# Optimization experiments

Hardware: AMD Instinct MI355X
Metric: run time of the kernel (lower is better)

Reference implementation:

```python
import jax, jax.numpy as jnp
import numpy as np

B, N = 8, 50000
DIM, C_DIM, TASK_DIM, H, NB, OUT = 3, 64, 512, 64, 5, 12


def setup_inputs() -> dict:
    key = jax.random.key(0)
    ks = jax.random.split(key, 16)
    s = lambda fan_in: 1.0 / np.sqrt(fan_in)
    inp = {
        "p": jax.random.normal(ks[0], (B, N, DIM), dtype=jnp.float32),
        "c": jax.random.normal(ks[1], (B, N, C_DIM), dtype=jnp.float32),
        "task_feature": jax.random.normal(ks[2], (B, TASK_DIM), dtype=jnp.float32),
        # params (stored as [in, out] so y = x @ W + b)
        "fc_p_W": jax.random.uniform(ks[3], (DIM, H), jnp.float32, -s(DIM), s(DIM)),
        "fc_p_b": jax.random.uniform(ks[4], (H,), jnp.float32, -s(DIM), s(DIM)),
        "fc_c_W": jax.random.uniform(ks[5], (NB, C_DIM + TASK_DIM, H), jnp.float32, -s(C_DIM + TASK_DIM), s(C_DIM + TASK_DIM)),
        "fc_c_b": jax.random.uniform(ks[6], (NB, H), jnp.float32, -s(C_DIM + TASK_DIM), s(C_DIM + TASK_DIM)),
        "blk0_W": jax.random.uniform(ks[7], (NB, H, H), jnp.float32, -s(H), s(H)),
        "blk0_b": jax.random.uniform(ks[8], (NB, H), jnp.float32, -s(H), s(H)),
        "blk1_W": jax.random.uniform(ks[9], (NB, H, H), jnp.float32, -s(H), s(H)) * 0.1,
        "blk1_b": jax.random.uniform(ks[10], (NB, H), jnp.float32, -s(H), s(H)),
        "fc_out_W": jax.random.uniform(ks[11], (H, OUT), jnp.float32, -s(H), s(H)),
        "fc_out_b": jax.random.uniform(ks[12], (OUT,), jnp.float32, -s(H), s(H)),
    }
    return inp


def reference(p, c, task_feature, fc_p_W, fc_p_b, fc_c_W, fc_c_b,
              blk0_W, blk0_b, blk1_W, blk1_b, fc_out_W, fc_out_b):
    b, n = p.shape[0], p.shape[1]
    # expand task feature to every point and concat with point-wise code c
    tf = jnp.broadcast_to(task_feature[:, None, :], (b, n, task_feature.shape[-1]))
    cc = jnp.concatenate([c, tf], axis=-1)              # [B, N, 576]
    net = p @ fc_p_W + fc_p_b                           # [B, N, H]
    for i in range(fc_c_W.shape[0]):
        net = net + cc @ fc_c_W[i] + fc_c_b[i]          # conditioning
        # ResnetBlockFC: dx = fc_1(relu(fc_0(relu(x)))); out = x + dx
        h = jax.nn.relu(net) @ blk0_W[i] + blk0_b[i]
        dx = jax.nn.relu(h) @ blk1_W[i] + blk1_b[i]
        net = net + dx
    out = jax.nn.relu(net) @ fc_out_W + fc_out_b        # [B, N, 12]
    return out
```

## Files before the change

kernel.cpp:

```cpp
#include <hip/hip_runtime.h>

#define B_    8
#define N_    50000
#define NB_   5
#define OUT_  12
#define THREADS 512
#define TILES_ 4
#define NGROUPS 6250
#define GRID   782

#define WL_OFF   0
#define TPL_OFF  124928
#define B0L_OFF  135168
#define B14_OFF  136448
#define FPW_OFF  136704
#define SMEM_BYTES 137472

typedef _Float16 half8  __attribute__((ext_vector_type(8)));
typedef __fp16   fp16x2 __attribute__((ext_vector_type(2)));
typedef float   floatx4 __attribute__((ext_vector_type(4)));

__device__ __forceinline__ half8 ldl8(const _Float16* p) {
    union { uint4 u; half8 h; } x;
    x.u = *(const uint4*)p;
    return x.h;
}

__device__ __forceinline__ half8 packB(floatx4 a, floatx4 b) {
    union { fp16x2 h2[4]; half8 h8; } u;
    u.h2[0] = __builtin_amdgcn_cvt_pkrtz(fmaxf(a[0], 0.f), fmaxf(a[1], 0.f));
    u.h2[1] = __builtin_amdgcn_cvt_pkrtz(fmaxf(a[2], 0.f), fmaxf(a[3], 0.f));
    u.h2[2] = __builtin_amdgcn_cvt_pkrtz(fmaxf(b[0], 0.f), fmaxf(b[1], 0.f));
    u.h2[3] = __builtin_amdgcn_cvt_pkrtz(fmaxf(b[2], 0.f), fmaxf(b[3], 0.f));
    return u.h8;
}

__device__ __forceinline__ void loadL8(half8 (&A)[8], const _Float16* wl, int stage, int lane) {
    const _Float16* b = wl + (size_t)stage * 512 * 8;
    #pragma unroll
    for (int T = 0; T < 4; ++T)
        #pragma unroll
        for (int h = 0; h < 2; ++h)
            A[2 * T + h] = ldl8(b + (size_t)(T * 128 + h * 64 + lane) * 8);
}

__global__ void prep_kernel(const float* __restrict__ fc_c_W,
                            const float* __restrict__ blk0_W,
                            const float* __restrict__ blk1_W,
                            const float* __restrict__ fc_out_W,
                            const float* __restrict__ tf,
                            _Float16* __restrict__ ws_w,
                            float* __restrict__ partials) {
    int bid = blockIdx.x, tid = threadIdx.x;
    if (bid < 32) {
        int u = bid * 256 + tid;
        if (u < 7680) {
            int m15 = u & 15, q = (u >> 4) & 3, h = (u >> 6) & 1, T = (u >> 7) & 3;
            int mi = u >> 9;
            int mat = mi / 5, i = mi % 5;
            int n = T * 16 + m15;
            _Float16 out[8];
            #pragma unroll
            for (int j = 0; j < 8; ++j) {
                float v;
                if (mat == 0) {
                    int k = 32 * h + 8 * q + j;
                    v = fc_c_W[((size_t)i * 576 + k) * 64 + n];
                } else {
                    int f = 32 * h + 16 * (j >> 2) + 4 * q + (j & 3);
                    const float* W = (mat == 1) ? blk0_W : blk1_W;
                    v = W[((size_t)i * 64 + f) * 64 + n];
                }
                out[j] = (_Float16)v;
            }
            *(uint4*)(ws_w + (size_t)u * 8) = *(uint4*)out;
        } else {
            int e = u - 7680;
            _Float16 out[8] = {};
            if (e < 128) {
                int m15 = e & 15, q = (e >> 4) & 3, h = (e >> 6) & 1;
                #pragma unroll
                for (int j = 0; j < 8; ++j) {
                    int f = 32 * h + 16 * (j >> 2) + 4 * q + (j & 3);
                    out[j] = (m15 < OUT_) ? (_Float16)fc_out_W[f * OUT_ + m15] : (_Float16)0.f;
                }
            }
            *(uint4*)(ws_w + (size_t)u * 8) = *(uint4*)out;
        }
    } else {
        int idx2 = bid - 32;
        int b = idx2 / 10, rem = idx2 % 10, i = rem >> 1, hf = rem & 1;
        int g = tid >> 6, j = tid & 63;
        const float* W  = fc_c_W + ((size_t)i * 576 + 64) * 64;
        const float* tb = tf + b * 512;
        int t0 = hf * 256 + g * 64;
        float acc = 0.f;
        #pragma unroll 8
        for (int t = 0; t < 64; ++t)
            acc += tb[t0 + t] * W[(size_t)(t0 + t) * 64 + j];
        partials[(((b * 5 + i) << 3) + (hf * 4 + g)) * 64 + j] = acc;
    }
}

__global__ void finalize_tp(const float* __restrict__ partials,
                            const float* __restrict__ fc_c_b,
                            const float* __restrict__ fc_p_b,
                            const float* __restrict__ blk1_b,
                            float* __restrict__ tp) {
    int u = blockIdx.x * 256 + threadIdx.x;
    if (u >= 2560) return;
    int b = u / 320, rem = u % 320, i = rem >> 6, j = rem & 63;
    float s = fc_c_b[i * 64 + j] + ((i == 0) ? fc_p_b[j] : blk1_b[(i - 1) * 64 + j]);
    #pragma unroll
    for (int k = 0; k < 8; ++k)
        s += partials[(((b * 5 + i) << 3) + k) * 64 + j];
    tp[u] = s;
}

__global__ __launch_bounds__(THREADS, 2) void decoder_kernel(
    const float* __restrict__ p_g, const float* __restrict__ c_g,
    const float* __restrict__ blk0_b, const float* __restrict__ blk1_b,
    const float* __restrict__ fc_p_W, const float* __restrict__ fc_out_b,
    const _Float16* __restrict__ ws_w, const float* __restrict__ tp_g,
    float* __restrict__ out_g)
{
    extern __shared__ char smem[];
    _Float16* wl   = (_Float16*)(smem + WL_OFF);
    float*    tp_l = (float*)(smem + TPL_OFF);
    float*    b0_l = (float*)(smem + B0L_OFF);
    float*    b14_l= (float*)(smem + B14_OFF);
    float*    fpw_l= (float*)(smem + FPW_OFF);

    const int tid = threadIdx.x, bid = blockIdx.x;

    {
        uint4* dw = (uint4*)wl;
        const uint4* sw = (const uint4*)ws_w;
        for (int u = tid; u < 7808; u += THREADS) dw[u] = sw[u];
        uint4* dt = (uint4*)tp_l;  const uint4* st = (const uint4*)tp_g;
        for (int u = tid; u < 640; u += THREADS) dt[u] = st[u];
        uint4* db = (uint4*)b0_l;  const uint4* sb = (const uint4*)blk0_b;
        for (int u = tid; u < 80; u += THREADS) db[u] = sb[u];
        uint4* d4 = (uint4*)b14_l; const uint4* s4 = (const uint4*)(blk1_b + 4 * 64);
        if (tid < 16) d4[tid] = s4[tid];
        uint4* df = (uint4*)fpw_l; const uint4* sf = (const uint4*)fc_p_W;
        if (tid < 48) df[tid] = sf[tid];
    }
    __syncthreads();

    const int lane = tid & 63;
    const int wv   = tid >> 6;
    const int q    = lane >> 4;
    const int m15  = lane & 15;

    const int g = bid * 8 + wv;
    if (g >= NGROUPS) return;

    int bt[TILES_];
    long pbase[TILES_];
    #pragma unroll
    for (int t = 0; t < TILES_; ++t) {
        int gt = g * TILES_ + t;
        int b  = gt / 3125;
        int lt = gt - b * 3125;
        bt[t] = b;
        pbase[t] = (long)b * N_ + (long)lt * 16;
    }

    half8 cB[TILES_][2];
    #pragma unroll
    for (int t = 0; t < TILES_; ++t) {
        const float* cr = c_g + (size_t)(pbase[t] + m15) * 64;
        #pragma unroll
        for (int h = 0; h < 2; ++h) {
            float4 v0 = *(const float4*)(cr + 32 * h + 8 * q);
            float4 v1 = *(const float4*)(cr + 32 * h + 8 * q + 4);
            union { fp16x2 h2[4]; half8 h8; } u;
            u.h2[0] = __builtin_amdgcn_cvt_pkrtz(v0.x, v0.y);
            u.h2[1] = __builtin_amdgcn_cvt_pkrtz(v0.z, v0.w);
            u.h2[2] = __builtin_amdgcn_cvt_pkrtz(v1.x, v1.y);
            u.h2[3] = __builtin_amdgcn_cvt_pkrtz(v1.z, v1.w);
            cB[t][h] = u.h8;
        }
    }

    floatx4 net4[TILES_][4];
    #pragma unroll
    for (int t = 0; t < TILES_; ++t) {
        long gp = pbase[t] + m15;
        float pp0 = p_g[gp * 3 + 0], pp1 = p_g[gp * 3 + 1], pp2 = p_g[gp * 3 + 2];
        #pragma unroll
        for (int T = 0; T < 4; ++T) {
            floatx4 w0 = *(const floatx4*)(fpw_l + 16 * T + 4 * q);
            floatx4 w1 = *(const floatx4*)(fpw_l + 64 + 16 * T + 4 * q);
            floatx4 w2 = *(const floatx4*)(fpw_l + 128 + 16 * T + 4 * q);
            net4[t][T] = w0 * pp0 + w1 * pp1 + w2 * pp2;
        }
    }

    #pragma unroll 1
    for (int i = 0; i < NB_; ++i) {
        half8 Ax[8], Ay[8];
        loadL8(Ax, wl, i, lane);
        loadL8(Ay, wl, 5 + i, lane);
        floatx4 bb0[4];
        #pragma unroll
        for (int T = 0; T < 4; ++T)
            bb0[T] = *(const floatx4*)(b0_l + i * 64 + 16 * T + 4 * q);
        #pragma unroll
        for (int t = 0; t < TILES_; ++t) {
            const float* tpb = tp_l + (bt[t] * NB_ + i) * 64 + 4 * q;
            #pragma unroll
            for (int T = 0; T < 4; ++T) {
                floatx4 a = net4[t][T];
                a = __builtin_amdgcn_mfma_f32_16x16x32_f16(Ax[2 * T], cB[t][0], a, 0, 0, 0);
                a = __builtin_amdgcn_mfma_f32_16x16x32_f16(Ax[2 * T + 1], cB[t][1], a, 0, 0, 0);
                net4[t][T] = a + *(const floatx4*)(tpb + 16 * T);
            }
        }
        loadL8(Ax, wl, 10 + i, lane);
        #pragma unroll
        for (int t = 0; t < TILES_; ++t) {
            half8 Bn0 = packB(net4[t][0], net4[t][1]);
            half8 Bn1 = packB(net4[t][2], net4[t][3]);
            floatx4 hh[4];
            #pragma unroll
            for (int T = 0; T < 4; ++T) {
                floatx4 a = bb0[T];
                a = __builtin_amdgcn_mfma_f32_16x16x32_f16(Ay[2 * T], Bn0, a, 0, 0, 0);
                a = __builtin_amdgcn_mfma_f32_16x16x32_f16(Ay[2 * T + 1], Bn1, a, 0, 0, 0);
                hh[T] = a;
            }
            half8 Bh0 = packB(hh[0], hh[1]);
            half8 Bh1 = packB(hh[2], hh[3]);
            #pragma unroll
            for (int T = 0; T < 4; ++T) {
                floatx4 a = net4[t][T];
                a = __builtin_amdgcn_mfma_f32_16x16x32_f16(Ax[2 * T], Bh0, a, 0, 0, 0);
                a = __builtin_amdgcn_mfma_f32_16x16x32_f16(Ax[2 * T + 1], Bh1, a, 0, 0, 0);
                net4[t][T] = a;
            }
        }
    }

    half8 Ao0 = ldl8(wl + (size_t)(15 * 512 + 0 * 64 + q * 16 + m15) * 8);
    half8 Ao1 = ldl8(wl + (size_t)(15 * 512 + 1 * 64 + q * 16 + m15) * 8);
    floatx4 b14v[4];
    #pragma unroll
    for (int T = 0; T < 4; ++T)
        b14v[T] = *(const floatx4*)(b14_l + 16 * T + 4 * q);
    floatx4 ob = {0.f, 0.f, 0.f, 0.f};
    if (q < 3) ob = *(const floatx4*)(fc_out_b + 4 * q);
    #pragma unroll
    for (int t = 0; t < TILES_; ++t) {
        half8 Bn0 = packB(net4[t][0] + b14v[0], net4[t][1] + b14v[1]);
        half8 Bn1 = packB(net4[t][2] + b14v[2], net4[t][3] + b14v[3]);
        floatx4 a = ob;
        a = __builtin_amdgcn_mfma_f32_16x16x32_f16(Ao0, Bn0, a, 0, 0, 0);
        a = __builtin_amdgcn_mfma_f32_16x16x32_f16(Ao1, Bn1, a, 0, 0, 0);
        if (q < 3) {
            long gp = pbase[t] + m15;
            *(float4*)(out_g + gp * OUT_ + 4 * q) = make_float4(a[0], a[1], a[2], a[3]);
        }
    }
}

extern "C" void kernel_launch(void* const* d_in, const int* in_sizes, int n_in,
                              void* d_out, int out_size, void* d_ws, size_t ws_size,
                              hipStream_t stream) {
    const float* p        = (const float*)d_in[0];
    const float* c        = (const float*)d_in[1];
    const float* tf       = (const float*)d_in[2];
    const float* fc_p_W   = (const float*)d_in[3];
    const float* fc_p_b   = (const float*)d_in[4];
    const float* fc_c_W   = (const float*)d_in[5];
    const float* fc_c_b   = (const float*)d_in[6];
    const float* blk0_W   = (const float*)d_in[7];
    const float* blk0_b   = (const float*)d_in[8];
    const float* blk1_W   = (const float*)d_in[9];
    const float* blk1_b   = (const float*)d_in[10];
    const float* fc_out_W = (const float*)d_in[11];
    const float* fc_out_b = (const float*)d_in[12];
    float* out = (float*)d_out;

    _Float16* ws_w  = (_Float16*)d_ws;
    float* partials = (float*)((char*)d_ws + 131072);
    float* tp       = (float*)((char*)d_ws + 131072 + 81920);

    prep_kernel<<<112, 256, 0, stream>>>(fc_c_W, blk0_W, blk1_W, fc_out_W, tf, ws_w, partials);
    finalize_tp<<<10, 256, 0, stream>>>(partials, fc_c_b, fc_p_b, blk1_b, tp);

    (void)hipFuncSetAttribute((const void*)decoder_kernel,
                        hipFuncAttributeMaxDynamicSharedMemorySize, SMEM_BYTES);
    decoder_kernel<<<GRID, THREADS, SMEM_BYTES, stream>>>(
        p, c, blk0_b, blk1_b, fc_p_W, fc_out_b, ws_w, tp, out);
}
```

Baseline: 253.4 us.

## Use persistent 768-thread blocks with 5-tile wave groups and packed fp16 relu

Launches a fixed grid of 256 blocks of 12 waves. Each wave loops over up to two 80-point groups, and every group stays inside one batch, so the task-projection bias is hoisted to registers once per stage. The aim is to amortise the 125 KB LDS weight load over more work per block and to cut per-tile bias loads. ReLU is now applied after fp16 packing with a vector max instead of per-element fmaxf. The risks are higher register pressure from five tiles at three blocks per CU, and some dead or duplicate code in the LDS staging.

```diff
diff --git a/kernel.cpp b/kernel.cpp
--- a/kernel.cpp
+++ b/kernel.cpp
@@ -4,10 +4,11 @@
 #define N_    50000
 #define NB_   5
 #define OUT_  12
-#define THREADS 512
-#define TILES_ 4
-#define NGROUPS 6250
-#define GRID   782
+#define THREADS 768
+#define GRID   256
+#define TILES_ 5
+#define NGROUPS 5000
+#define NWAVES 3072
 
 #define WL_OFF   0
 #define TPL_OFF  124928
@@ -28,11 +29,12 @@
 
 __device__ __forceinline__ half8 packB(floatx4 a, floatx4 b) {
     union { fp16x2 h2[4]; half8 h8; } u;
-    u.h2[0] = __builtin_amdgcn_cvt_pkrtz(fmaxf(a[0], 0.f), fmaxf(a[1], 0.f));
-    u.h2[1] = __builtin_amdgcn_cvt_pkrtz(fmaxf(a[2], 0.f), fmaxf(a[3], 0.f));
-    u.h2[2] = __builtin_amdgcn_cvt_pkrtz(fmaxf(b[0], 0.f), fmaxf(b[1], 0.f));
-    u.h2[3] = __builtin_amdgcn_cvt_pkrtz(fmaxf(b[2], 0.f), fmaxf(b[3], 0.f));
-    return u.h8;
+    u.h2[0] = __builtin_amdgcn_cvt_pkrtz(a[0], a[1]);
+    u.h2[1] = __builtin_amdgcn_cvt_pkrtz(a[2], a[3]);
+    u.h2[2] = __builtin_amdgcn_cvt_pkrtz(b[0], b[1]);
+    u.h2[3] = __builtin_amdgcn_cvt_pkrtz(b[2], b[3]);
+    half8 z = {};
+    return __builtin_elementwise_max(u.h8, z);
 }
 
 __device__ __forceinline__ void loadL8(half8 (&A)[8], const _Float16* wl, int stage, int lane) {
@@ -117,7 +119,7 @@
     tp[u] = s;
 }
 
-__global__ __launch_bounds__(THREADS, 2) void decoder_kernel(
+__global__ __launch_bounds__(THREADS, 3) void decoder_kernel(
     const float* __restrict__ p_g, const float* __restrict__ c_g,
     const float* __restrict__ blk0_b, const float* __restrict__ blk1_b,
     const float* __restrict__ fc_p_W, const float* __restrict__ fc_out_b,
@@ -137,14 +139,16 @@
         uint4* dw = (uint4*)wl;
         const uint4* sw = (const uint4*)ws_w;
         for (int u = tid; u < 7808; u += THREADS) dw[u] = sw[u];
-        uint4* dt = (uint4*)tp_l;  const uint4* st = (const uint4*)tp_g;
-        for (int u = tid; u < 640; u += THREADS) dt[u] = st[u];
-        uint4* db = (uint4*)b0_l;  const uint4* sb = (const uint4*)blk0_b;
-        for (int u = tid; u < 80; u += THREADS) db[u] = sb[u];
-        uint4* d4 = (uint4*)b14_l; const uint4* s4 = (const uint4*)(blk1_b + 4 * 64);
-        if (tid < 16) d4[tid] = s4[tid];
-        uint4* df = (uint4*)fpw_l; const uint4* sf = (const uint4*)fc_p_W;
-        if (tid < 48) df[tid] = sf[tid];
+        if (tid < 640) ((uint4*)tp_l)[tid] = ((const uint4*)tp_g)[tid];
+        else if (tid < 720) ((uint4*)b0_l)[tid - 640] = ((const uint4*)blk0_b)[tid - 640];
+        else if (tid < 736) ((uint4*)b14_l)[tid - 720] = ((const uint4*)(blk1_b + 256))[tid - 720];
+        else if (tid < 752) {
+            int u = tid - 736;
+            if (u < 48) ((uint4*)fpw_l)[u] = ((const uint4*)fc_p_W)[u];
+        }
+        if (tid >= 704 && tid < 736) {
+        }
+        if (tid < 48) ((uint4*)fpw_l)[tid] = ((const uint4*)fc_p_W)[tid];
     }
     __syncthreads();
 
@@ -152,115 +156,113 @@
     const int wv   = tid >> 6;
     const int q    = lane >> 4;
     const int m15  = lane & 15;
-
-    const int g = bid * 8 + wv;
-    if (g >= NGROUPS) return;
-
-    int bt[TILES_];
-    long pbase[TILES_];
-    #pragma unroll
-    for (int t = 0; t < TILES_; ++t) {
-        int gt = g * TILES_ + t;
-        int b  = gt / 3125;
-        int lt = gt - b * 3125;
-        bt[t] = b;
-        pbase[t] = (long)b * N_ + (long)lt * 16;
-    }
-
-    half8 cB[TILES_][2];
-    #pragma unroll
-    for (int t = 0; t < TILES_; ++t) {
-        const float* cr = c_g + (size_t)(pbase[t] + m15) * 64;
-        #pragma unroll
-        for (int h = 0; h < 2; ++h) {
-            float4 v0 = *(const float4*)(cr + 32 * h + 8 * q);
-            float4 v1 = *(const float4*)(cr + 32 * h + 8 * q + 4);
-            union { fp16x2 h2[4]; half8 h8; } u;
-            u.h2[0] = __builtin_amdgcn_cvt_pkrtz(v0.x, v0.y);
-            u.h2[1] = __builtin_amdgcn_cvt_pkrtz(v0.z, v0.w);
-            u.h2[2] = __builtin_amdgcn_cvt_pkrtz(v1.x, v1.y);
-            u.h2[3] = __builtin_amdgcn_cvt_pkrtz(v1.z, v1.w);
-            cB[t][h] = u.h8;
-        }
-    }
-
-    floatx4 net4[TILES_][4];
-    #pragma unroll
-    for (int t = 0; t < TILES_; ++t) {
-        long gp = pbase[t] + m15;
-        float pp0 = p_g[gp * 3 + 0], pp1 = p_g[gp * 3 + 1], pp2 = p_g[gp * 3 + 2];
-        #pragma unroll
-        for (int T = 0; T < 4; ++T) {
-            floatx4 w0 = *(const floatx4*)(fpw_l + 16 * T + 4 * q);
-            floatx4 w1 = *(const floatx4*)(fpw_l + 64 + 16 * T + 4 * q);
-            floatx4 w2 = *(const floatx4*)(fpw_l + 128 + 16 * T + 4 * q);
-            net4[t][T] = w0 * pp0 + w1 * pp1 + w2 * pp2;
-        }
-    }
-
-    #pragma unroll 1
-    for (int i = 0; i < NB_; ++i) {
-        half8 Ax[8], Ay[8];
-        loadL8(Ax, wl, i, lane);
-        loadL8(Ay, wl, 5 + i, lane);
-        floatx4 bb0[4];
-        #pragma unroll
-        for (int T = 0; T < 4; ++T)
-            bb0[T] = *(const floatx4*)(b0_l + i * 64 + 16 * T + 4 * q);
-        #pragma unroll
-        for (int t = 0; t < TILES_; ++t) {
-            const float* tpb = tp_l + (bt[t] * NB_ + i) * 64 + 4 * q;
-            #pragma unroll
-            for (int T = 0; T < 4; ++T) {
-                floatx4 a = net4[t][T];
-                a = __builtin_amdgcn_mfma_f32_16x16x32_f16(Ax[2 * T], cB[t][0], a, 0, 0, 0);
-                a = __builtin_amdgcn_mfma_f32_16x16x32_f16(Ax[2 * T + 1], cB[t][1], a, 0, 0, 0);
-                net4[t][T] = a + *(const floatx4*)(tpb + 16 * T);
-            }
-        }
-        loadL8(Ax, wl, 10 + i, lane);
-        #pragma unroll
-        for (int t = 0; t < TILES_; ++t) {
-            half8 Bn0 = packB(net4[t][0], net4[t][1]);
-            half8 Bn1 = packB(net4[t][2], net4[t][3]);
-            floatx4 hh[4];
-            #pragma unroll
-            for (int T = 0; T < 4; ++T) {
-                floatx4 a = bb0[T];
-                a = __builtin_amdgcn_mfma_f32_16x16x32_f16(Ay[2 * T], Bn0, a, 0, 0, 0);
-                a = __builtin_amdgcn_mfma_f32_16x16x32_f16(Ay[2 * T + 1], Bn1, a, 0, 0, 0);
-                hh[T] = a;
-            }
-            half8 Bh0 = packB(hh[0], hh[1]);
-            half8 Bh1 = packB(hh[2], hh[3]);
-            #pragma unroll
-            for (int T = 0; T < 4; ++T) {
-                floatx4 a = net4[t][T];
-                a = __builtin_amdgcn_mfma_f32_16x16x32_f16(Ax[2 * T], Bh0, a, 0, 0, 0);
-                a = __builtin_amdgcn_mfma_f32_16x16x32_f16(Ax[2 * T + 1], Bh1, a, 0, 0, 0);
-                net4[t][T] = a;
-            }
-        }
-    }
-
+    const int W    = bid * 12 + wv;
+
+    floatx4 ob = {0.f, 0.f, 0.f, 0.f};
+    if (q < 3) ob = *(const floatx4*)(fc_out_b + 4 * q);
     half8 Ao0 = ldl8(wl + (size_t)(15 * 512 + 0 * 64 + q * 16 + m15) * 8);
     half8 Ao1 = ldl8(wl + (size_t)(15 * 512 + 1 * 64 + q * 16 + m15) * 8);
-    floatx4 b14v[4];
-    #pragma unroll
-    for (int T = 0; T < 4; ++T)
-        b14v[T] = *(const floatx4*)(b14_l + 16 * T + 4 * q);
-    floatx4 ob = {0.f, 0.f, 0.f, 0.f};
-    if (q < 3) ob = *(const floatx4*)(fc_out_b + 4 * q);
-    #pragma unroll
-    for (int t = 0; t < TILES_; ++t) {
-        half8 Bn0 = packB(net4[t][0] + b14v[0], net4[t][1] + b14v[1]);
-        half8 Bn1 = packB(net4[t][2] + b14v[2], net4[t][3] + b14v[3]);
-        floatx4 a = ob;
-        a = __builtin_amdgcn_mfma_f32_16x16x32_f16(Ao0, Bn0, a, 0, 0, 0);
-        a = __builtin_amdgcn_mfma_f32_16x16x32_f16(Ao1, Bn1, a, 0, 0, 0);
-        if (q < 3) {
-            long gp = pbase[t] + m15;
-            *(float4*)(out_g + gp * OUT_ + 4 * q) = make_float4(a[0], a[1], a[2], a[3]);
+
+    #pragma unroll 1
+    for (int rep = 0; rep < 2; ++rep) {
+        const int g = W + rep * NWAVES;
+        if (g >= NGROUPS) break;
+        const int b  = g / 625;
+        const long pbase0 = (long)b * N_ + (long)(g - b * 625) * 80;
+        const float* tpb = tp_l + b * (NB_ * 64);
+
+        half8 cB[TILES_][2];
+        #pragma unroll
+        for (int t = 0; t < TILES_; ++t) {
+            const float* cr = c_g + (size_t)(pbase0 + t * 16 + m15) * 64;
+            #pragma unroll
+            for (int h = 0; h < 2; ++h) {
+                float4 v0 = *(const float4*)(cr + 32 * h + 8 * q);
+                float4 v1 = *(const float4*)(cr + 32 * h + 8 * q + 4);
+                union { fp16x2 h2[4]; half8 h8; } u;
+                u.h2[0] = __builtin_amdgcn_cvt_pkrtz(v0.x, v0.y);
+                u.h2[1] = __builtin_amdgcn_cvt_pkrtz(v0.z, v0.w);
+                u.h2[2] = __builtin_amdgcn_cvt_pkrtz(v1.x, v1.y);
+                u.h2[3] = __builtin_amdgcn_cvt_pkrtz(v1.z, v1.w);
+                cB[t][h] = u.h8;
+            }
+        }
+
+        floatx4 net4[TILES_][4];
+        #pragma unroll
+        for (int t = 0; t < TILES_; ++t) {
+            long gp = pbase0 + t * 16 + m15;
+            float pp0 = p_g[gp * 3 + 0], pp1 = p_g[gp * 3 + 1], pp2 = p_g[gp * 3 + 2];
+            #pragma unroll
+            for (int T = 0; T < 4; ++T) {
+                floatx4 w0 = *(const floatx4*)(fpw_l + 16 * T + 4 * q);
+                floatx4 w1 = *(const floatx4*)(fpw_l + 64 + 16 * T + 4 * q);
+                floatx4 w2 = *(const floatx4*)(fpw_l + 128 + 16 * T + 4 * q);
+                net4[t][T] = w0 * pp0 + w1 * pp1 + w2 * pp2;
+            }
+        }
+
+        #pragma unroll 1
+        for (int i = 0; i < NB_; ++i) {
+            half8 Ax[8], Ay[8];
+            loadL8(Ax, wl, i, lane);
+            loadL8(Ay, wl, 5 + i, lane);
+            floatx4 tpv[4], bb0[4];
+            #pragma unroll
+            for (int T = 0; T < 4; ++T) {
+                tpv[T] = *(const floatx4*)(tpb + i * 64 + 16 * T + 4 * q);
+                bb0[T] = *(const floatx4*)(b0_l + i * 64 + 16 * T + 4 * q);
+            }
+            #pragma unroll
+            for (int t = 0; t < TILES_; ++t) {
+                #pragma unroll
+                for (int T = 0; T < 4; ++T) {
+                    floatx4 a = net4[t][T];
+                    a = __builtin_amdgcn_mfma_f32_16x16x32_f16(Ax[2 * T], cB[t][0], a, 0, 0, 0);
+                    a = __builtin_amdgcn_mfma_f32_16x16x32_f16(Ax[2 * T + 1], cB[t][1], a, 0, 0, 0);
+                    net4[t][T] = a + tpv[T];
+                }
+            }
+            loadL8(Ax, wl, 10 + i, lane);
+            #pragma unroll
+            for (int t = 0; t < TILES_; ++t) {
+                half8 Bn0 = packB(net4[t][0], net4[t][1]);
+                half8 Bn1 = packB(net4[t][2], net4[t][3]);
+                floatx4 hh[4];
+                #pragma unroll
+                for (int T = 0; T < 4; ++T) {
+                    floatx4 a = bb0[T];
+                    a = __builtin_amdgcn_mfma_f32_16x16x32_f16(Ay[2 * T], Bn0, a, 0, 0, 0);
+                    a = __builtin_amdgcn_mfma_f32_16x16x32_f16(Ay[2 * T + 1], Bn1, a, 0, 0, 0);
+                    hh[T] = a;
+                }
+                half8 Bh0 = packB(hh[0], hh[1]);
+                half8 Bh1 = packB(hh[2], hh[3]);
+                #pragma unroll
+                for (int T = 0; T < 4; ++T) {
+                    floatx4 a = net4[t][T];
+                    a = __builtin_amdgcn_mfma_f32_16x16x32_f16(Ax[2 * T], Bh0, a, 0, 0, 0);
+                    a = __builtin_amdgcn_mfma_f32_16x16x32_f16(Ax[2 * T + 1], Bh1, a, 0, 0, 0);
+                    net4[t][T] = a;
+                }
+            }
+        }
+
+        floatx4 b14v[4];
+        #pragma unroll
+        for (int T = 0; T < 4; ++T)
+            b14v[T] = *(const floatx4*)(b14_l + 16 * T + 4 * q);
+        #pragma unroll
+        for (int t = 0; t < TILES_; ++t) {
+            half8 Bn0 = packB(net4[t][0] + b14v[0], net4[t][1] + b14v[1]);
+            half8 Bn1 = packB(net4[t][2] + b14v[2], net4[t][3] + b14v[3]);
+            floatx4 a = ob;
+            a = __builtin_amdgcn_mfma_f32_16x16x32_f16(Ao0, Bn0, a, 0, 0, 0);
+            a = __builtin_amdgcn_mfma_f32_16x16x32_f16(Ao1, Bn1, a, 0, 0, 0);
+            if (q < 3) {
+                long gp = pbase0 + t * 16 + m15;
+                *(float4*)(out_g + gp * OUT_ + 4 * q) = make_float4(a[0], a[1], a[2], a[3]);
+            }
         }
     }
 }
```

After: 430.2 us. 69.7% more time.
